# Kernel optimization log

Hardware: AMD Instinct MI355X
Metric: run time of the kernel (lower is better)

## Reference

```python
import math
import jax, jax.numpy as jnp
import numpy as np

B, P, L, R = 16, 256, 8, 128  # n_embd = L*R = 1024
H = 4 * L * R                 # MLP hidden = 4096

def new_gelu(x):
    # tanh-approx GELU as in NewGELU
    c = math.sqrt(2.0 / math.pi)
    return 0.5 * x * (1.0 + jnp.tanh(c * (x + 0.044715 * x * x * x)))

def setup_inputs() -> dict:
    key = jax.random.key(0)
    k1, k2, k3 = jax.random.split(key, 3)
    x = jax.random.normal(k1, (B, P, L, R), dtype=jnp.float32)
    W1 = jax.random.normal(k2, (L * R, H), dtype=jnp.float32) * 0.02
    b1 = jnp.zeros((H,), dtype=jnp.float32)
    W2 = jax.random.normal(k3, (H, R), dtype=jnp.float32) * 0.02
    b2 = jnp.zeros((R,), dtype=jnp.float32)
    return {"x": x, "W1": W1, "b1": b1, "W2": W2, "b2": b2}

def reference(x, W1, b1, W2, b2):
    b, p, l, r = x.shape
    flat = x.reshape(b, p, l * r)                       # [B,P,L*R]
    # Level i input = flat with first i*R entries zeroed (zeros-pad + tail slice)
    col = jnp.arange(l * r)
    mask = (col[None, :] >= (jnp.arange(l) * r)[:, None]).astype(x.dtype)  # [L, L*R]
    inp = flat[:, :, None, :] * mask                    # [B,P,L,L*R]
    h = new_gelu(jnp.einsum('bple,eh->bplh', inp, W1) + b1)  # [B,P,L,H]
    out = jnp.einsum('bplh,hr->bplr', h, W2) + b2       # [B,P,L,R]
    return out
```

## Files before the change

### kernel.cpp

```cpp
#include <hip/hip_runtime.h>
#include <hip/hip_bf16.h>


typedef _Float16 half8 __attribute__((ext_vector_type(8)));
typedef _Float16 half4 __attribute__((ext_vector_type(4)));
typedef _Float16 half2v __attribute__((ext_vector_type(2)));
typedef __fp16   fp16x2 __attribute__((ext_vector_type(2)));
typedef float    f32x4  __attribute__((ext_vector_type(4)));
typedef float    f32x16 __attribute__((ext_vector_type(16)));

#define MFMA3216(A,B,C) __builtin_amdgcn_mfma_f32_32x32x16_f16(A, B, C, 0, 0, 0)

__device__ __forceinline__ float gelu_f(float x){
  float t2 = x * fmaf(x*x, -0.10294324f, -2.30220842f);
  float e  = __builtin_amdgcn_exp2f(t2);
  return x * __builtin_amdgcn_rcpf(1.0f + e);
}

#define XROW 1028
#define W1ROW 258
#define W2ROW 130

__global__ void k_prep(const float* __restrict__ x, const float* __restrict__ w1,
                       const float* __restrict__ w2,
                       _Float16* __restrict__ xt, _Float16* __restrict__ w1t,
                       _Float16* __restrict__ w2t){
  __shared__ _Float16 Xs[32*XROW];
  int bid = blockIdx.x;
  int t   = threadIdx.x;
  if (bid < 128){
    const float4* x4 = reinterpret_cast<const float4*>(x) + (size_t)bid*8192;
    #pragma unroll
    for (int i = 0; i < 32; ++i){
      float4 v = x4[i*256 + t];
      half4 h;
      h[0]=(_Float16)v.x; h[1]=(_Float16)v.y; h[2]=(_Float16)v.z; h[3]=(_Float16)v.w;
      *reinterpret_cast<half4*>(Xs + i*XROW + t*4) = h;
    }
    __syncthreads();
    #pragma unroll
    for (int f = 0; f < 16; ++f){
      int fragidx = f*256 + t;
      int lane = fragidx & 63, kf = fragidx >> 6;
      int tok32 = lane & 31;
      int k = kf*16 + (lane >> 5)*8;
      half8 v = *reinterpret_cast<const half8*>(Xs + tok32*XROW + k);
      *reinterpret_cast<half8*>(xt + ((size_t)bid*4096 + fragidx)*8) = v;
    }
  } else if (bid < 1152){
    int bid2 = bid - 128;
    int kf = bid2 >> 4, ng = bid2 & 15;
    _Float16* Ws = Xs;
    const float4* w1f4 = reinterpret_cast<const float4*>(w1);
    #pragma unroll
    for (int q = 0; q < 4; ++q){
      int idx = q*256 + t;
      int row = idx >> 6, col4 = idx & 63;
      float4 v = w1f4[(size_t)(kf*16 + row)*1024 + ng*64 + col4];
      half4 h;
      h[0]=(_Float16)v.x; h[1]=(_Float16)v.y; h[2]=(_Float16)v.z; h[3]=(_Float16)v.w;
      *reinterpret_cast<half4*>(Ws + row*W1ROW + col4*4) = h;
    }
    __syncthreads();
    int hq = ng >> 1;
    #pragma unroll
    for (int e = 0; e < 2; ++e){
      int fl = e*256 + t;
      int lane = fl & 63, htl = fl >> 6;
      int ht = (ng & 1)*8 + htl;
      int r0 = (lane >> 5)*8, c = htl*32 + (lane & 31);
      half8 v;
      #pragma unroll
      for (int j = 0; j < 8; ++j) v[j] = Ws[(r0 + j)*W1ROW + c];
      *reinterpret_cast<half8*>(
          w1t + ((size_t)hq*65536 + (size_t)kf*1024 + ht*64 + lane)*8) = v;
    }
  } else {
    int bid3 = bid - 1152;
    int hq = bid3 >> 5, kf = bid3 & 31;
    _Float16* Ws = Xs;
    const float4* w2f4 = reinterpret_cast<const float4*>(w2);
    #pragma unroll
    for (int q = 0; q < 2; ++q){
      int idx = q*256 + t;
      int row = idx >> 5, col4 = idx & 31;
      float4 v = w2f4[(size_t)(hq*512 + kf*16 + row)*32 + col4];
      half4 h;
      h[0]=(_Float16)v.x; h[1]=(_Float16)v.y; h[2]=(_Float16)v.z; h[3]=(_Float16)v.w;
      *reinterpret_cast<half4*>(Ws + row*W2ROW + col4*4) = h;
    }
    __syncthreads();
    int lane = t & 63, rt = t >> 6;
    int r0 = (lane >> 5)*8, c = rt*32 + (lane & 31);
    half8 v;
    #pragma unroll
    for (int j = 0; j < 8; ++j) v[j] = Ws[(r0 + j)*W2ROW + c];
    *reinterpret_cast<half8*>(
        w2t + (((size_t)(hq*32 + kf)*4 + rt)*512 + (size_t)lane*8)) = v;
  }
}

__global__ void k_init_out(const float* __restrict__ b2, float* __restrict__ out){
  int i = blockIdx.x*256 + threadIdx.x;
  float4 bv = reinterpret_cast<const float4*>(b2)[i & 31];
  reinterpret_cast<float4*>(out)[i] = bv;
}

__global__ void k_reduce(const unsigned* __restrict__ part, const float* __restrict__ b2,
                         float* __restrict__ out){
  int tid = blockIdx.x*256 + threadIdx.x;
  int r   = tid & 127;
  int tc  = (tid >> 7) & 31;
  int j   = (tid >> 12) & 7;
  int tt  = tid >> 15;
  float s0 = 0.f, s1 = 0.f;
  #pragma unroll
  for (int hq = 0; hq < 8; ++hq){
    unsigned v = __builtin_nontemporal_load(part + (size_t)hq*2097152 + tid);
    half2v h = __builtin_bit_cast(half2v, v);
    s0 += (float)h[0];
    s1 += (float)h[1];
  }
  int tka = tt*64 + (tc >> 3)*16 + (tc & 7);
  float bb = b2[r];
  out[(size_t)tka*1024 + j*128 + r]       = s0 + bb;
  out[(size_t)(tka+8)*1024 + j*128 + r]   = s1 + bb;
}

__global__ __launch_bounds__(768, 3) void k_treemlp(
    const _Float16* __restrict__ xt, const _Float16* __restrict__ w1t,
    const _Float16* __restrict__ w2t, const float* __restrict__ b1,
    unsigned* __restrict__ partial, float* __restrict__ out, int use_partial){
  int b    = blockIdx.x;
  int hq   = b & 7;
  int tt   = b >> 3;
  int t    = threadIdx.x;
  int w    = t >> 6;
  int lane = t & 63;
  int t32 = lane & 31, q2 = lane >> 5;

  __shared__ _Float16 Pbuf[2][32768];
  __shared__ _Float16 Xls[2][8192];

  f32x16 acc1[2][2];
  if (w < 8){
    #pragma unroll
    for (int hf = 0; hf < 2; ++hf){
      int base = hq*512 + (w*2 + hf)*32;
      #pragma unroll
      for (int g = 0; g < 4; ++g){
        float4 bv = *reinterpret_cast<const float4*>(b1 + base + 8*g + 4*q2);
        #pragma unroll
        for (int c = 0; c < 4; ++c){
          acc1[hf][0][g*4 + c] = ((const float*)&bv)[c];
          acc1[hf][1][g*4 + c] = ((const float*)&bv)[c];
        }
      }
    }
    #pragma unroll
    for (int c = 0; c < 2; ++c){
      int idx = c*512 + (w*64 + lane);
      int lane_s = idx & 63, s = (idx >> 6) & 7, tgl = idx >> 9;
      half8 v = *reinterpret_cast<const half8*>(
          xt + (size_t)((tt*2 + tgl)*64 + 7*8 + s)*512 + lane_s*8);
      *reinterpret_cast<half8*>(&Xls[1][(size_t)idx*8]) = v;
    }
  }
  __syncthreads();

  const _Float16* w1base = w1t + (size_t)hq*524288 + (size_t)(w*2)*512 + lane*8;
  int rt = w - 8;
  const _Float16* w2base = w2t + ((size_t)(hq*32)*4 + rt)*512 + lane*8;

  #pragma unroll
  for (int k = 0; k < 9; ++k){
    if (w < 8){
      if (k <= 7){
        int L = 7 - k;
        if (L >= 1){
          #pragma unroll
          for (int c = 0; c < 2; ++c){
            int idx = c*512 + (w*64 + lane);
            int lane_s = idx & 63, s = (idx >> 6) & 7, tgl = idx >> 9;
            half8 v = *reinterpret_cast<const half8*>(
                xt + (size_t)((tt*2 + tgl)*64 + (L-1)*8 + s)*512 + lane_s*8);
            *reinterpret_cast<half8*>(&Xls[(L-1) & 1][(size_t)idx*8]) = v;
          }
        }
        const _Float16* xb = Xls[L & 1];
        #pragma unroll
        for (int c2 = 0; c2 < 2; ++c2){
          half8 af[8];
          #pragma unroll
          for (int u = 0; u < 4; ++u){
            int kfg = L*8 + c2*4 + u;
            af[u*2    ] = *reinterpret_cast<const half8*>(w1base + (size_t)(kfg*16    )*512);
            af[u*2 + 1] = *reinterpret_cast<const half8*>(w1base + (size_t)(kfg*16 + 1)*512);
          }
          #pragma unroll
          for (int u = 0; u < 4; ++u){
            int s = c2*4 + u;
            half8 x0 = *reinterpret_cast<const half8*>(&xb[(size_t)((    s)*64 + lane)*8]);
            half8 x1 = *reinterpret_cast<const half8*>(&xb[(size_t)((8 + s)*64 + lane)*8]);
            acc1[0][0] = MFMA3216(af[u*2    ], x0, acc1[0][0]);
            acc1[0][1] = MFMA3216(af[u*2    ], x1, acc1[0][1]);
            acc1[1][0] = MFMA3216(af[u*2 + 1], x0, acc1[1][0]);
            acc1[1][1] = MFMA3216(af[u*2 + 1], x1, acc1[1][1]);
          }
        }
        _Float16* pb = Pbuf[L & 1];
        #pragma unroll
        for (int hf = 0; hf < 2; ++hf)
          #pragma unroll
          for (int tg = 0; tg < 2; ++tg)
            #pragma unroll
            for (int g2 = 0; g2 < 4; ++g2){
              fp16x2 lo = __builtin_amdgcn_cvt_pkrtz(
                  gelu_f(acc1[hf][tg][g2*4 + 0]), gelu_f(acc1[hf][tg][g2*4 + 1]));
              fp16x2 hi = __builtin_amdgcn_cvt_pkrtz(
                  gelu_f(acc1[hf][tg][g2*4 + 2]), gelu_f(acc1[hf][tg][g2*4 + 3]));
              half4 hv;
              hv[0]=(_Float16)lo[0]; hv[1]=(_Float16)lo[1];
              hv[2]=(_Float16)hi[0]; hv[3]=(_Float16)hi[1];
              int kf = (w*2 + hf)*2 + (g2 >> 1);
              *reinterpret_cast<half4*>(
                  &pb[(size_t)((tg*32 + kf)*64 + t32 + 32*(g2 & 1))*8 + 4*q2]) = hv;
            }
      }
    } else {
      if (k >= 1){
        int Lc = 8 - k;
        const _Float16* pb = Pbuf[Lc & 1];
        f32x16 o0, o1;
        #pragma unroll
        for (int c = 0; c < 16; ++c){ o0[c] = 0.f; o1[c] = 0.f; }
        #pragma unroll
        for (int c4 = 0; c4 < 4; ++c4){
          half8 wfb[8];
          #pragma unroll
          for (int u = 0; u < 8; ++u)
            wfb[u] = *reinterpret_cast<const half8*>(w2base + (size_t)(c4*8 + u)*2048);
          #pragma unroll
          for (int u = 0; u < 8; ++u){
            int kf = c4*8 + u;
            half8 p0 = *reinterpret_cast<const half8*>(&pb[(size_t)((     kf)*64 + lane)*8]);
            half8 p1 = *reinterpret_cast<const half8*>(&pb[(size_t)((32 + kf)*64 + lane)*8]);
            o0 = MFMA3216(p0, wfb[u], o0);
            o1 = MFMA3216(p1, wfb[u], o1);
          }
        }
        if (use_partial){
          unsigned* pbase = partial + (size_t)hq*2097152 + (size_t)tt*32768
                          + (size_t)Lc*4096;
          #pragma unroll
          for (int th = 0; th < 2; ++th){
            const f32x16& oJ = th ? o1 : o0;
            #pragma unroll
            for (int i = 0; i < 8; ++i){
              int gg = i >> 2, ii = i & 3;
              int lo = gg*8 + ii;
              fp16x2 p = __builtin_amdgcn_cvt_pkrtz(oJ[lo], oJ[lo + 4]);
              int tc = (th*2 + gg)*8 + ii + 4*q2;
              __builtin_nontemporal_store(__builtin_bit_cast(unsigned, p),
                                          pbase + (size_t)tc*128 + rt*32 + t32);
            }
          }
        } else {
          #pragma unroll
          for (int th = 0; th < 2; ++th){
            const f32x16& oJ = th ? o1 : o0;
            #pragma unroll
            for (int reg = 0; reg < 16; ++reg){
              int tok = tt*64 + th*32 + (reg & 3) + 8*(reg >> 2) + 4*q2;
              atomicAdd(out + (size_t)tok*1024 + Lc*128 + rt*32 + t32, oJ[reg]);
            }
          }
        }
      }
    }
    __syncthreads();
  }
}

extern "C" void kernel_launch(void* const* d_in, const int* in_sizes, int n_in,
                              void* d_out, int out_size, void* d_ws, size_t ws_size,
                              hipStream_t stream){
  (void)in_sizes; (void)n_in; (void)out_size;
  const float* x  = (const float*)d_in[0];
  const float* W1 = (const float*)d_in[1];
  const float* b1 = (const float*)d_in[2];
  const float* W2 = (const float*)d_in[3];
  const float* b2 = (const float*)d_in[4];
  float* out = (float*)d_out;

  _Float16* xt  = (_Float16*)d_ws;
  _Float16* w1t = xt  + 4194304;
  _Float16* w2t = w1t + 4194304;
  unsigned* partial = (unsigned*)(w2t + 524288);
  const size_t need = (size_t)(4194304 + 4194304 + 524288)*2 + (size_t)16777216*4;
  int use_partial = (ws_size >= need) ? 1 : 0;

  hipLaunchKernelGGL(k_prep, dim3(1408), dim3(256), 0, stream, x, W1, W2, xt, w1t, w2t);
  if (!use_partial)
    hipLaunchKernelGGL(k_init_out, dim3(4096), dim3(256), 0, stream, b2, out);
  hipLaunchKernelGGL(k_treemlp, dim3(512), dim3(768), 0, stream,
                     xt, w1t, w2t, b1, partial, out, use_partial);
  if (use_partial)
    hipLaunchKernelGGL(k_reduce, dim3(8192), dim3(256), 0, stream, partial, b2, out);
}
```

Measured before the change: 197.5 us.

## Single-buffer LDS staging with extra barrier to raise occupancy of tree-MLP kernel

Replaces the double-buffered Pbuf and Xls shared arrays with single buffers, which halves LDS use. Launch bounds go from 3 to 6 blocks per CU. GELU write-back to Pbuf and the prefetch of the next X slice now run in a new phase after a barrier, followed by a second barrier, so the producer and consumer warps no longer overlap within a step. The goal is higher occupancy to hide latency, at the cost of an extra synchronisation per iteration, serialised producer and consumer stages, and tighter register limits.

```diff
diff --git a/kernel.cpp b/kernel.cpp
--- a/kernel.cpp
+++ b/kernel.cpp
@@ -127,7 +127,7 @@
   out[(size_t)(tka+8)*1024 + j*128 + r]   = s1 + bb;
 }
 
-__global__ __launch_bounds__(768, 3) void k_treemlp(
+__global__ __launch_bounds__(768, 6) void k_treemlp(
     const _Float16* __restrict__ xt, const _Float16* __restrict__ w1t,
     const _Float16* __restrict__ w2t, const float* __restrict__ b1,
     unsigned* __restrict__ partial, float* __restrict__ out, int use_partial){
@@ -139,8 +139,8 @@
   int lane = t & 63;
   int t32 = lane & 31, q2 = lane >> 5;
 
-  __shared__ _Float16 Pbuf[2][32768];
-  __shared__ _Float16 Xls[2][8192];
+  __shared__ _Float16 Pbuf[32768];
+  __shared__ _Float16 Xls[8192];
 
   f32x16 acc1[2][2];
   if (w < 8){
@@ -163,7 +163,7 @@
       int lane_s = idx & 63, s = (idx >> 6) & 7, tgl = idx >> 9;
       half8 v = *reinterpret_cast<const half8*>(
           xt + (size_t)((tt*2 + tgl)*64 + 7*8 + s)*512 + lane_s*8);
-      *reinterpret_cast<half8*>(&Xls[1][(size_t)idx*8]) = v;
+      *reinterpret_cast<half8*>(&Xls[(size_t)idx*8]) = v;
     }
   }
   __syncthreads();
@@ -177,17 +177,7 @@
     if (w < 8){
       if (k <= 7){
         int L = 7 - k;
-        if (L >= 1){
-          #pragma unroll
-          for (int c = 0; c < 2; ++c){
-            int idx = c*512 + (w*64 + lane);
-            int lane_s = idx & 63, s = (idx >> 6) & 7, tgl = idx >> 9;
-            half8 v = *reinterpret_cast<const half8*>(
-                xt + (size_t)((tt*2 + tgl)*64 + (L-1)*8 + s)*512 + lane_s*8);
-            *reinterpret_cast<half8*>(&Xls[(L-1) & 1][(size_t)idx*8]) = v;
-          }
-        }
-        const _Float16* xb = Xls[L & 1];
+        const _Float16* xb = Xls;
         #pragma unroll
         for (int c2 = 0; c2 < 2; ++c2){
           half8 af[8];
@@ -208,29 +198,11 @@
             acc1[1][1] = MFMA3216(af[u*2 + 1], x1, acc1[1][1]);
           }
         }
-        _Float16* pb = Pbuf[L & 1];
-        #pragma unroll
-        for (int hf = 0; hf < 2; ++hf)
-          #pragma unroll
-          for (int tg = 0; tg < 2; ++tg)
-            #pragma unroll
-            for (int g2 = 0; g2 < 4; ++g2){
-              fp16x2 lo = __builtin_amdgcn_cvt_pkrtz(
-                  gelu_f(acc1[hf][tg][g2*4 + 0]), gelu_f(acc1[hf][tg][g2*4 + 1]));
-              fp16x2 hi = __builtin_amdgcn_cvt_pkrtz(
-                  gelu_f(acc1[hf][tg][g2*4 + 2]), gelu_f(acc1[hf][tg][g2*4 + 3]));
-              half4 hv;
-              hv[0]=(_Float16)lo[0]; hv[1]=(_Float16)lo[1];
-              hv[2]=(_Float16)hi[0]; hv[3]=(_Float16)hi[1];
-              int kf = (w*2 + hf)*2 + (g2 >> 1);
-              *reinterpret_cast<half4*>(
-                  &pb[(size_t)((tg*32 + kf)*64 + t32 + 32*(g2 & 1))*8 + 4*q2]) = hv;
-            }
       }
     } else {
       if (k >= 1){
         int Lc = 8 - k;
-        const _Float16* pb = Pbuf[Lc & 1];
+        const _Float16* pbc = Pbuf;
         f32x16 o0, o1;
         #pragma unroll
         for (int c = 0; c < 16; ++c){ o0[c] = 0.f; o1[c] = 0.f; }
@@ -243,8 +215,8 @@
           #pragma unroll
           for (int u = 0; u < 8; ++u){
             int kf = c4*8 + u;
-            half8 p0 = *reinterpret_cast<const half8*>(&pb[(size_t)((     kf)*64 + lane)*8]);
-            half8 p1 = *reinterpret_cast<const half8*>(&pb[(size_t)((32 + kf)*64 + lane)*8]);
+            half8 p0 = *reinterpret_cast<const half8*>(&pbc[(size_t)((     kf)*64 + lane)*8]);
+            half8 p1 = *reinterpret_cast<const half8*>(&pbc[(size_t)((32 + kf)*64 + lane)*8]);
             o0 = MFMA3216(p0, wfb[u], o0);
             o1 = MFMA3216(p1, wfb[u], o1);
           }
@@ -279,6 +251,48 @@
       }
     }
     __syncthreads();
+    if (w < 8 && k <= 7){
+      int L = 7 - k;
+      half8 v0, v1;
+      int idx0 = 0, idx1 = 0;
+      if (L >= 1){
+        idx0 = (w*64 + lane);
+        idx1 = 512 + (w*64 + lane);
+        {
+          int lane_s = idx0 & 63, s = (idx0 >> 6) & 7, tgl = idx0 >> 9;
+          v0 = *reinterpret_cast<const half8*>(
+              xt + (size_t)((tt*2 + tgl)*64 + (L-1)*8 + s)*512 + lane_s*8);
+        }
+        {
+          int lane_s = idx1 & 63, s = (idx1 >> 6) & 7, tgl = idx1 >> 9;
+          v1 = *reinterpret_cast<const half8*>(
+              xt + (size_t)((tt*2 + tgl)*64 + (L-1)*8 + s)*512 + lane_s*8);
+        }
+      }
+      _Float16* pb = Pbuf;
+      #pragma unroll
+      for (int hf = 0; hf < 2; ++hf)
+        #pragma unroll
+        for (int tg = 0; tg < 2; ++tg)
+          #pragma unroll
+          for (int g2 = 0; g2 < 4; ++g2){
+            fp16x2 lo = __builtin_amdgcn_cvt_pkrtz(
+                gelu_f(acc1[hf][tg][g2*4 + 0]), gelu_f(acc1[hf][tg][g2*4 + 1]));
+            fp16x2 hi = __builtin_amdgcn_cvt_pkrtz(
+                gelu_f(acc1[hf][tg][g2*4 + 2]), gelu_f(acc1[hf][tg][g2*4 + 3]));
+            half4 hv;
+            hv[0]=(_Float16)lo[0]; hv[1]=(_Float16)lo[1];
+            hv[2]=(_Float16)hi[0]; hv[3]=(_Float16)hi[1];
+            int kf = (w*2 + hf)*2 + (g2 >> 1);
+            *reinterpret_cast<half4*>(
+                &pb[(size_t)((tg*32 + kf)*64 + t32 + 32*(g2 & 1))*8 + 4*q2]) = hv;
+          }
+      if (L >= 1){
+        *reinterpret_cast<half8*>(&Xls[(size_t)idx0*8]) = v0;
+        *reinterpret_cast<half8*>(&Xls[(size_t)idx1*8]) = v1;
+      }
+    }
+    __syncthreads();
   }
 }
 
```

Measured after the change: 743.1 us. 276% more time.

## Halve token tile per block and rebalance warps to doubled grid

Applied to the files above, without the earlier changes.

Each block of the fused MLP kernel now covers 32 tokens instead of 64 and runs 6 warps instead of 12. The grid doubles to 1024 blocks. GEMM1 warps each own 4 hidden-column tiles and GEMM2 warps each own 2 output-column tiles, and the reduce kernel's indexing is adjusted to match. Shared memory per block is halved, which should allow more resident blocks and better occupancy. The cost is less reuse of each W1/W2 fragment loaded from global memory, since every weight fragment now feeds half as many tokens, so weight traffic doubles.

```diff
diff --git a/kernel.cpp b/kernel.cpp
--- a/kernel.cpp
+++ b/kernel.cpp
@@ -110,9 +110,9 @@
                          float* __restrict__ out){
   int tid = blockIdx.x*256 + threadIdx.x;
   int r   = tid & 127;
-  int tc  = (tid >> 7) & 31;
-  int j   = (tid >> 12) & 7;
-  int tt  = tid >> 15;
+  int tc  = (tid >> 7) & 15;
+  int j   = (tid >> 11) & 7;
+  int tt  = tid >> 14;
   float s0 = 0.f, s1 = 0.f;
   #pragma unroll
   for (int hq = 0; hq < 8; ++hq){
@@ -121,13 +121,13 @@
     s0 += (float)h[0];
     s1 += (float)h[1];
   }
-  int tka = tt*64 + (tc >> 3)*16 + (tc & 7);
+  int tka = tt*32 + (tc >> 3)*16 + (tc & 7);
   float bb = b2[r];
   out[(size_t)tka*1024 + j*128 + r]       = s0 + bb;
   out[(size_t)(tka+8)*1024 + j*128 + r]   = s1 + bb;
 }
 
-__global__ __launch_bounds__(768, 3) void k_treemlp(
+__global__ __launch_bounds__(384, 3) void k_treemlp(
     const _Float16* __restrict__ xt, const _Float16* __restrict__ w1t,
     const _Float16* __restrict__ w2t, const float* __restrict__ b1,
     unsigned* __restrict__ partial, float* __restrict__ out, int use_partial){
@@ -139,140 +139,139 @@
   int lane = t & 63;
   int t32 = lane & 31, q2 = lane >> 5;
 
-  __shared__ _Float16 Pbuf[2][32768];
-  __shared__ _Float16 Xls[2][8192];
-
-  f32x16 acc1[2][2];
-  if (w < 8){
-    #pragma unroll
-    for (int hf = 0; hf < 2; ++hf){
-      int base = hq*512 + (w*2 + hf)*32;
+  __shared__ _Float16 Pbuf[2][16384];
+  __shared__ _Float16 Xls[2][4096];
+
+  f32x16 acc1[4];
+  if (w < 4){
+    #pragma unroll
+    for (int hf = 0; hf < 4; ++hf){
+      int base = hq*512 + (w*4 + hf)*32;
       #pragma unroll
       for (int g = 0; g < 4; ++g){
         float4 bv = *reinterpret_cast<const float4*>(b1 + base + 8*g + 4*q2);
-        #pragma unroll
-        for (int c = 0; c < 4; ++c){
-          acc1[hf][0][g*4 + c] = ((const float*)&bv)[c];
-          acc1[hf][1][g*4 + c] = ((const float*)&bv)[c];
-        }
+        acc1[hf][g*4 + 0] = bv.x; acc1[hf][g*4 + 1] = bv.y;
+        acc1[hf][g*4 + 2] = bv.z; acc1[hf][g*4 + 3] = bv.w;
       }
     }
     #pragma unroll
     for (int c = 0; c < 2; ++c){
-      int idx = c*512 + (w*64 + lane);
-      int lane_s = idx & 63, s = (idx >> 6) & 7, tgl = idx >> 9;
+      int idx = c*256 + w*64 + lane;
+      int lane_s = idx & 63, s = idx >> 6;
       half8 v = *reinterpret_cast<const half8*>(
-          xt + (size_t)((tt*2 + tgl)*64 + 7*8 + s)*512 + lane_s*8);
+          xt + (size_t)(tt*64 + 7*8 + s)*512 + lane_s*8);
       *reinterpret_cast<half8*>(&Xls[1][(size_t)idx*8]) = v;
     }
   }
   __syncthreads();
 
-  const _Float16* w1base = w1t + (size_t)hq*524288 + (size_t)(w*2)*512 + lane*8;
-  int rt = w - 8;
-  const _Float16* w2base = w2t + ((size_t)(hq*32)*4 + rt)*512 + lane*8;
+  const _Float16* w1base = w1t + (size_t)hq*524288 + (size_t)(w*4)*512 + lane*8;
+  int rtb = (w - 4)*2;
+  const _Float16* w2base = w2t + (size_t)(hq*128 + rtb)*512 + lane*8;
 
   #pragma unroll
   for (int k = 0; k < 9; ++k){
-    if (w < 8){
+    if (w < 4){
       if (k <= 7){
         int L = 7 - k;
         if (L >= 1){
           #pragma unroll
           for (int c = 0; c < 2; ++c){
-            int idx = c*512 + (w*64 + lane);
-            int lane_s = idx & 63, s = (idx >> 6) & 7, tgl = idx >> 9;
+            int idx = c*256 + w*64 + lane;
+            int lane_s = idx & 63, s = idx >> 6;
             half8 v = *reinterpret_cast<const half8*>(
-                xt + (size_t)((tt*2 + tgl)*64 + (L-1)*8 + s)*512 + lane_s*8);
+                xt + (size_t)(tt*64 + (L-1)*8 + s)*512 + lane_s*8);
             *reinterpret_cast<half8*>(&Xls[(L-1) & 1][(size_t)idx*8]) = v;
           }
         }
         const _Float16* xb = Xls[L & 1];
         #pragma unroll
-        for (int c2 = 0; c2 < 2; ++c2){
+        for (int c2 = 0; c2 < 4; ++c2){
           half8 af[8];
           #pragma unroll
-          for (int u = 0; u < 4; ++u){
-            int kfg = L*8 + c2*4 + u;
-            af[u*2    ] = *reinterpret_cast<const half8*>(w1base + (size_t)(kfg*16    )*512);
-            af[u*2 + 1] = *reinterpret_cast<const half8*>(w1base + (size_t)(kfg*16 + 1)*512);
-          }
-          #pragma unroll
-          for (int u = 0; u < 4; ++u){
-            int s = c2*4 + u;
-            half8 x0 = *reinterpret_cast<const half8*>(&xb[(size_t)((    s)*64 + lane)*8]);
-            half8 x1 = *reinterpret_cast<const half8*>(&xb[(size_t)((8 + s)*64 + lane)*8]);
-            acc1[0][0] = MFMA3216(af[u*2    ], x0, acc1[0][0]);
-            acc1[0][1] = MFMA3216(af[u*2    ], x1, acc1[0][1]);
-            acc1[1][0] = MFMA3216(af[u*2 + 1], x0, acc1[1][0]);
-            acc1[1][1] = MFMA3216(af[u*2 + 1], x1, acc1[1][1]);
+          for (int u = 0; u < 2; ++u){
+            int kfg = L*8 + c2*2 + u;
+            #pragma unroll
+            for (int hf = 0; hf < 4; ++hf)
+              af[u*4 + hf] = *reinterpret_cast<const half8*>(
+                  w1base + (size_t)kfg*8192 + hf*512);
+          }
+          #pragma unroll
+          for (int u = 0; u < 2; ++u){
+            int s = c2*2 + u;
+            half8 x0 = *reinterpret_cast<const half8*>(&xb[(size_t)(s*64 + lane)*8]);
+            #pragma unroll
+            for (int hf = 0; hf < 4; ++hf)
+              acc1[hf] = MFMA3216(af[u*4 + hf], x0, acc1[hf]);
           }
         }
         _Float16* pb = Pbuf[L & 1];
         #pragma unroll
-        for (int hf = 0; hf < 2; ++hf)
-          #pragma unroll
-          for (int tg = 0; tg < 2; ++tg)
-            #pragma unroll
-            for (int g2 = 0; g2 < 4; ++g2){
-              fp16x2 lo = __builtin_amdgcn_cvt_pkrtz(
-                  gelu_f(acc1[hf][tg][g2*4 + 0]), gelu_f(acc1[hf][tg][g2*4 + 1]));
-              fp16x2 hi = __builtin_amdgcn_cvt_pkrtz(
-                  gelu_f(acc1[hf][tg][g2*4 + 2]), gelu_f(acc1[hf][tg][g2*4 + 3]));
-              half4 hv;
-              hv[0]=(_Float16)lo[0]; hv[1]=(_Float16)lo[1];
-              hv[2]=(_Float16)hi[0]; hv[3]=(_Float16)hi[1];
-              int kf = (w*2 + hf)*2 + (g2 >> 1);
-              *reinterpret_cast<half4*>(
-                  &pb[(size_t)((tg*32 + kf)*64 + t32 + 32*(g2 & 1))*8 + 4*q2]) = hv;
-            }
+        for (int hf = 0; hf < 4; ++hf)
+          #pragma unroll
+          for (int g2 = 0; g2 < 4; ++g2){
+            fp16x2 lo = __builtin_amdgcn_cvt_pkrtz(
+                gelu_f(acc1[hf][g2*4 + 0]), gelu_f(acc1[hf][g2*4 + 1]));
+            fp16x2 hi = __builtin_amdgcn_cvt_pkrtz(
+                gelu_f(acc1[hf][g2*4 + 2]), gelu_f(acc1[hf][g2*4 + 3]));
+            int kf = (w*4 + hf)*2 + (g2 >> 1);
+            uint2 uv;
+            uv.x = __builtin_bit_cast(unsigned, lo);
+            uv.y = __builtin_bit_cast(unsigned, hi);
+            *reinterpret_cast<uint2*>(
+                &pb[(size_t)((kf*64 + t32 + 32*(g2 & 1)))*8 + 4*q2]) = uv;
+          }
       }
     } else {
       if (k >= 1){
         int Lc = 8 - k;
-        const _Float16* pb = Pbuf[Lc & 1];
+        const _Float16* pbc = Pbuf[Lc & 1];
         f32x16 o0, o1;
         #pragma unroll
         for (int c = 0; c < 16; ++c){ o0[c] = 0.f; o1[c] = 0.f; }
         #pragma unroll
-        for (int c4 = 0; c4 < 4; ++c4){
+        for (int c4 = 0; c4 < 8; ++c4){
           half8 wfb[8];
           #pragma unroll
-          for (int u = 0; u < 8; ++u)
-            wfb[u] = *reinterpret_cast<const half8*>(w2base + (size_t)(c4*8 + u)*2048);
-          #pragma unroll
-          for (int u = 0; u < 8; ++u){
-            int kf = c4*8 + u;
-            half8 p0 = *reinterpret_cast<const half8*>(&pb[(size_t)((     kf)*64 + lane)*8]);
-            half8 p1 = *reinterpret_cast<const half8*>(&pb[(size_t)((32 + kf)*64 + lane)*8]);
-            o0 = MFMA3216(p0, wfb[u], o0);
-            o1 = MFMA3216(p1, wfb[u], o1);
+          for (int u = 0; u < 4; ++u){
+            wfb[u*2    ] = *reinterpret_cast<const half8*>(
+                w2base + (size_t)(c4*4 + u)*2048);
+            wfb[u*2 + 1] = *reinterpret_cast<const half8*>(
+                w2base + (size_t)(c4*4 + u)*2048 + 512);
+          }
+          #pragma unroll
+          for (int u = 0; u < 4; ++u){
+            int kf = c4*4 + u;
+            half8 p = *reinterpret_cast<const half8*>(&pbc[(size_t)(kf*64 + lane)*8]);
+            o0 = MFMA3216(p, wfb[u*2    ], o0);
+            o1 = MFMA3216(p, wfb[u*2 + 1], o1);
           }
         }
         if (use_partial){
-          unsigned* pbase = partial + (size_t)hq*2097152 + (size_t)tt*32768
-                          + (size_t)Lc*4096;
-          #pragma unroll
-          for (int th = 0; th < 2; ++th){
-            const f32x16& oJ = th ? o1 : o0;
+          unsigned* pbase = partial + (size_t)hq*2097152 + (size_t)tt*16384
+                          + (size_t)Lc*2048;
+          #pragma unroll
+          for (int rt2 = 0; rt2 < 2; ++rt2){
+            const f32x16& oJ = rt2 ? o1 : o0;
             #pragma unroll
             for (int i = 0; i < 8; ++i){
               int gg = i >> 2, ii = i & 3;
               int lo = gg*8 + ii;
               fp16x2 p = __builtin_amdgcn_cvt_pkrtz(oJ[lo], oJ[lo + 4]);
-              int tc = (th*2 + gg)*8 + ii + 4*q2;
+              int tc = gg*8 + ii + 4*q2;
               __builtin_nontemporal_store(__builtin_bit_cast(unsigned, p),
-                                          pbase + (size_t)tc*128 + rt*32 + t32);
+                  pbase + (size_t)tc*128 + (rtb + rt2)*32 + t32);
             }
           }
         } else {
           #pragma unroll
-          for (int th = 0; th < 2; ++th){
-            const f32x16& oJ = th ? o1 : o0;
+          for (int rt2 = 0; rt2 < 2; ++rt2){
+            const f32x16& oJ = rt2 ? o1 : o0;
             #pragma unroll
             for (int reg = 0; reg < 16; ++reg){
-              int tok = tt*64 + th*32 + (reg & 3) + 8*(reg >> 2) + 4*q2;
-              atomicAdd(out + (size_t)tok*1024 + Lc*128 + rt*32 + t32, oJ[reg]);
+              int tok = tt*32 + (reg & 3) + 8*(reg >> 2) + 4*q2;
+              atomicAdd(out + (size_t)tok*1024 + Lc*128 + (rtb + rt2)*32 + t32,
+                        oJ[reg]);
             }
           }
         }
@@ -303,7 +302,7 @@
   hipLaunchKernelGGL(k_prep, dim3(1408), dim3(256), 0, stream, x, W1, W2, xt, w1t, w2t);
   if (!use_partial)
     hipLaunchKernelGGL(k_init_out, dim3(4096), dim3(256), 0, stream, b2, out);
-  hipLaunchKernelGGL(k_treemlp, dim3(512), dim3(768), 0, stream,
+  hipLaunchKernelGGL(k_treemlp, dim3(1024), dim3(384), 0, stream,
                      xt, w1t, w2t, b1, partial, out, use_partial);
   if (use_partial)
     hipLaunchKernelGGL(k_reduce, dim3(8192), dim3(256), 0, stream, partial, b2, out);
```

Result: slower. 276.0 us (+39.7%).
